# Performance work log

Hardware: AMD Instinct MI355X
Metric: run time of the kernel (lower is better)

Reference implementation:

```python
import jax, jax.numpy as jnp
import numpy as np

N_NODES = 50000
N_EDGES = 400000


def setup_inputs() -> dict:
    key = jax.random.key(0)
    ks = jax.random.split(key, 8)
    d_in, d_hid, d_out = 512, 512, 256
    feats = jax.random.normal(ks[0], (N_NODES, d_in), dtype=jnp.float32)
    src = jax.random.randint(ks[1], (N_EDGES,), 0, N_NODES, dtype=jnp.int32)
    dst = jax.random.randint(ks[2], (N_EDGES,), 0, N_NODES, dtype=jnp.int32)
    # Glorot-ish scaled weights so activations stay O(1)
    W0 = jax.random.normal(ks[3], (d_in, d_hid), dtype=jnp.float32) / np.sqrt(d_in)
    b0 = jnp.zeros((d_hid,), jnp.float32)
    W1 = jax.random.normal(ks[4], (d_hid, d_hid), dtype=jnp.float32) / np.sqrt(d_hid)
    b1 = jnp.zeros((d_hid,), jnp.float32)
    W2 = jax.random.normal(ks[5], (d_hid, d_out), dtype=jnp.float32) / np.sqrt(d_hid)
    b2 = jnp.zeros((d_out,), jnp.float32)
    return {"feats": feats, "src": src, "dst": dst,
            "W0": W0, "b0": b0, "W1": W1, "b1": b1, "W2": W2, "b2": b2}


def _sage_conv_gcn(h, src, dst, W, b, deg):
    # DGL SAGEConv aggregator_type='gcn':
    # h_neigh[v] = (sum_{u->v} h[u] + h[v]) / (in_deg(v) + 1); out = h_neigh @ W + b
    agg = jax.ops.segment_sum(h[src], dst, num_segments=h.shape[0])  # [N, d]
    h_neigh = (agg + h) / (deg[:, None] + 1.0)
    return h_neigh @ W + b


def reference(feats, src, dst, W0, b0, W1, b1, W2, b2):
    N = feats.shape[0]
    deg = jax.ops.segment_sum(jnp.ones((src.shape[0],), feats.dtype), dst,
                              num_segments=N)  # in-degree per node
    h = jax.nn.relu(_sage_conv_gcn(feats, src, dst, W0, b0, deg))  # dropout p=0, norm none
    h = jax.nn.relu(_sage_conv_gcn(h, src, dst, W1, b1, deg))
    h = _sage_conv_gcn(h, src, dst, W2, b2, deg)  # final layer: no activation
    return h
```

## Files before the change

kernel.cpp:

```cpp
#include <hip/hip_runtime.h>
#include <stdint.h>

#define N_NODES 50000
#define N_EDGES 400000
#define MPAD    50048
#define SCAN_B  49

typedef __bf16 bf16x8 __attribute__((ext_vector_type(8)));
typedef float  f32x4  __attribute__((ext_vector_type(4)));
typedef unsigned short ushort_t;
typedef unsigned int   uint_t;

__device__ __forceinline__ ushort_t f2b(float f){
    uint_t x = __float_as_uint(f);
    x += 0x7FFFu + ((x >> 16) & 1u);
    return (ushort_t)(x >> 16);
}
__device__ __forceinline__ float b2f(ushort_t h){
    return __uint_as_float(((uint_t)h) << 16);
}

__device__ __forceinline__ int xcd_swz(int orig, int nwg){
    int q = nwg >> 3, r = nwg & 7;
    int xcd = orig & 7, idx = orig >> 3;
    int base = (xcd < r) ? xcd * (q + 1) : r * (q + 1) + (xcd - r) * q;
    return base + idx;
}

__global__ void zero_two(int* a, int* b, int n){
    int i = blockIdx.x * blockDim.x + threadIdx.x;
    if (i < n){ a[i] = 0; b[i] = 0; }
}

__global__ void hist_kernel(const int* __restrict__ dst, int* __restrict__ deg, int E){
    int i = blockIdx.x * blockDim.x + threadIdx.x;
    if (i < E) atomicAdd(&deg[dst[i]], 1);
}

__global__ __launch_bounds__(1024) void blk_scan_kernel(
        const int* __restrict__ deg, int* __restrict__ offs,
        int* __restrict__ bsum, int n){
    __shared__ int buf[1024];
    const int t = threadIdx.x, b = blockIdx.x;
    const int i = b * 1024 + t;
    int v = (i < n) ? deg[i] : 0;
    buf[t] = v; __syncthreads();
    for (int off = 1; off < 1024; off <<= 1){
        int x = (t >= off) ? buf[t - off] : 0;
        __syncthreads();
        buf[t] += x;
        __syncthreads();
    }
    if (i < n) offs[i] = buf[t] - v;
    if (t == 1023) bsum[b] = buf[1023];
}

__global__ void bsum_scan_kernel(int* __restrict__ bsum, int nb){
    int t = threadIdx.x;
    int orig = (t < nb) ? bsum[t] : 0;
    int v = orig;
    #pragma unroll
    for (int off = 1; off < 64; off <<= 1){
        int x = __shfl_up(v, off, 64);
        if (t >= off) v += x;
    }
    if (t < nb) bsum[t] = v - orig;
}

__global__ __launch_bounds__(1024) void add_off_kernel(
        int* __restrict__ offs, const int* __restrict__ bsum, int n){
    int i = blockIdx.x * 1024 + threadIdx.x;
    if (i < n) offs[i] += bsum[blockIdx.x];
    if (i == 0) offs[n] = N_EDGES;
}

__global__ void fill_kernel(const int* __restrict__ src, const int* __restrict__ dst,
                            const int* __restrict__ offs, int* __restrict__ cursor,
                            int* __restrict__ nbr, int E){
    int i = blockIdx.x * blockDim.x + threadIdx.x;
    if (i < E){
        int d = dst[i];
        int p = atomicAdd(&cursor[d], 1);
        nbr[offs[d] + p] = src[i];
    }
}

__global__ void wtrans_kernel(const float* __restrict__ W, ushort_t* __restrict__ Wt,
                              int K, int N){
    int i = blockIdx.x * blockDim.x + threadIdx.x;
    if (i < K * N){
        int n = i / K, k = i - n * K;
        Wt[i] = f2b(W[k * N + n]);
    }
}

__device__ __forceinline__ void load16(const void* g, void* l){
    __builtin_amdgcn_global_load_lds((const __attribute__((address_space(1))) void*)g,
                                     (__attribute__((address_space(3))) void*)l, 16, 0, 0);
}

__global__ __launch_bounds__(256, 4) void gemm128_bt(const ushort_t* __restrict__ A,
                                                     const ushort_t* __restrict__ Bt,
                                                     ushort_t* __restrict__ C,
                                                     int NBN, int N, int K){
    __shared__ ushort_t As[128 * 64];
    __shared__ ushort_t Bs[128 * 64];
    const int tid  = threadIdx.x, lane = tid & 63, wave = tid >> 6;
    const int wg = xcd_swz(blockIdx.x, gridDim.x);
    const int bm = wg / NBN, bn = wg - bm * NBN;
    const int fr = lane & 15;
    const int wm = (wave >> 1) * 64, wn = (wave & 1) * 64;
    f32x4 acc[4][4] = {};

    for (int kt = 0; kt < K; kt += 64){
        __syncthreads();
        #pragma unroll
        for (int i = 0; i < 4; i++){
            int s = tid + i * 256;
            int row = s >> 3, p = s & 7, c = p ^ (row & 7);
            load16(A + (size_t)(bm * 128 + row) * K + kt + c * 8,
                   (char*)As + s * 16);
        }
        #pragma unroll
        for (int i = 0; i < 4; i++){
            int s = tid + i * 256;
            int row = s >> 3, p = s & 7, c = p ^ (row & 7);
            load16(Bt + (size_t)(bn * 128 + row) * K + kt + c * 8,
                   (char*)Bs + s * 16);
        }
        __syncthreads();
        #pragma unroll
        for (int ks = 0; ks < 2; ks++){
            const int c = (lane >> 4) + ks * 4;
            const int cx = c ^ (fr & 7);
            bf16x8 af[4], bf[4];
            #pragma unroll
            for (int t = 0; t < 4; t++)
                af[t] = *(const bf16x8*)(const void*)(As + (wm + t * 16 + fr) * 64 + cx * 8);
            #pragma unroll
            for (int t = 0; t < 4; t++)
                bf[t] = *(const bf16x8*)(const void*)(Bs + (wn + t * 16 + fr) * 64 + cx * 8);
            #pragma unroll
            for (int tm = 0; tm < 4; tm++)
                #pragma unroll
                for (int tn = 0; tn < 4; tn++)
                    acc[tm][tn] = __builtin_amdgcn_mfma_f32_16x16x32_bf16(
                                      af[tm], bf[tn], acc[tm][tn], 0, 0, 0);
        }
    }
    const int r0 = (lane >> 4) * 4, c0 = lane & 15;
    #pragma unroll
    for (int tm = 0; tm < 4; tm++){
        #pragma unroll
        for (int tn = 0; tn < 4; tn++){
            int rbase = bm * 128 + wm + tm * 16 + r0;
            int cidx  = bn * 128 + wn + tn * 16 + c0;
            #pragma unroll
            for (int reg = 0; reg < 4; reg++)
                C[(size_t)(rbase + reg) * N + cidx] = f2b(acc[tm][tn][reg]);
        }
    }
}

__global__ __launch_bounds__(256, 3) void gemm128_a32(const float* __restrict__ A,
                                                      const ushort_t* __restrict__ Bt,
                                                      ushort_t* __restrict__ C,
                                                      int K){
    __shared__ ushort_t As[128 * 64];
    __shared__ ushort_t Bs[128 * 64];
    const int tid  = threadIdx.x, lane = tid & 63, wave = tid >> 6;
    const int wg = xcd_swz(blockIdx.x, gridDim.x);
    const int bm = wg >> 2, bn = wg & 3;
    const int fr = lane & 15;
    const int wm = (wave >> 1) * 64, wn = (wave & 1) * 64;
    f32x4 acc[4][4] = {};

    for (int kt = 0; kt < K; kt += 64){
        __syncthreads();
        float4 x[4], y[4];
        #pragma unroll
        for (int i = 0; i < 4; i++){
            int s = tid + i * 256;
            int row = s >> 3, p = s & 7, c = p ^ (row & 7);
            int grow = bm * 128 + row;
            if (grow < N_NODES){
                const float* pp = A + (size_t)grow * K + kt + c * 8;
                x[i] = *(const float4*)(const void*)pp;
                y[i] = *(const float4*)(const void*)(pp + 4);
            } else {
                x[i] = make_float4(0.f, 0.f, 0.f, 0.f);
                y[i] = make_float4(0.f, 0.f, 0.f, 0.f);
            }
        }
        #pragma unroll
        for (int i = 0; i < 4; i++){
            int s = tid + i * 256;
            int row = s >> 3, p = s & 7, c = p ^ (row & 7);
            load16(Bt + (size_t)(bn * 128 + row) * K + kt + c * 8,
                   (char*)Bs + s * 16);
        }
        #pragma unroll
        for (int i = 0; i < 4; i++){
            int s = tid + i * 256;
            uint4 o;
            o.x = (uint_t)f2b(x[i].x) | ((uint_t)f2b(x[i].y) << 16);
            o.y = (uint_t)f2b(x[i].z) | ((uint_t)f2b(x[i].w) << 16);
            o.z = (uint_t)f2b(y[i].x) | ((uint_t)f2b(y[i].y) << 16);
            o.w = (uint_t)f2b(y[i].z) | ((uint_t)f2b(y[i].w) << 16);
            *(uint4*)(void*)((char*)As + s * 16) = o;
        }
        __syncthreads();
        #pragma unroll
        for (int ks = 0; ks < 2; ks++){
            const int c = (lane >> 4) + ks * 4;
            const int cx = c ^ (fr & 7);
            bf16x8 af[4], bf[4];
            #pragma unroll
            for (int t = 0; t < 4; t++)
                af[t] = *(const bf16x8*)(const void*)(As + (wm + t * 16 + fr) * 64 + cx * 8);
            #pragma unroll
            for (int t = 0; t < 4; t++)
                bf[t] = *(const bf16x8*)(const void*)(Bs + (wn + t * 16 + fr) * 64 + cx * 8);
            #pragma unroll
            for (int tm = 0; tm < 4; tm++)
                #pragma unroll
                for (int tn = 0; tn < 4; tn++)
                    acc[tm][tn] = __builtin_amdgcn_mfma_f32_16x16x32_bf16(
                                      af[tm], bf[tn], acc[tm][tn], 0, 0, 0);
        }
    }
    const int r0 = (lane >> 4) * 4, c0 = lane & 15;
    #pragma unroll
    for (int tm = 0; tm < 4; tm++){
        #pragma unroll
        for (int tn = 0; tn < 4; tn++){
            int rbase = bm * 128 + wm + tm * 16 + r0;
            int cidx  = bn * 128 + wn + tn * 16 + c0;
            #pragma unroll
            for (int reg = 0; reg < 4; reg++)
                C[(size_t)(rbase + reg) * 512 + cidx] = f2b(acc[tm][tn][reg]);
        }
    }
}

__device__ __forceinline__ void acc4(float* a, uint2 y){
    a[0] += b2f((ushort_t)(y.x & 0xffff)); a[1] += b2f((ushort_t)(y.x >> 16));
    a[2] += b2f((ushort_t)(y.y & 0xffff)); a[3] += b2f((ushort_t)(y.y >> 16));
}

__global__ __launch_bounds__(512) void agg_relu_kernel(
        const ushort_t* __restrict__ Y, const int* __restrict__ offs,
        const int* __restrict__ nbr, const float* __restrict__ bias,
        ushort_t* __restrict__ H){
    const int lane = threadIdx.x & 63, wv = threadIdx.x >> 6;
    const int v   = blockIdx.x * 4 + (wv >> 1);
    const int off = (wv & 1) * 256 + lane * 4;
    float a[4];
    {   uint2 y = *(const uint2*)(const void*)(Y + (size_t)v * 512 + off);
        a[0] = b2f((ushort_t)(y.x & 0xffff)); a[1] = b2f((ushort_t)(y.x >> 16));
        a[2] = b2f((ushort_t)(y.y & 0xffff)); a[3] = b2f((ushort_t)(y.y >> 16)); }
    const int beg = offs[v], end = offs[v + 1];
    int i = beg;
    for (; i + 8 <= end; i += 8){
        uint2 yy[8];
        #pragma unroll
        for (int j = 0; j < 8; j++){
            int u = nbr[i + j];
            yy[j] = *(const uint2*)(const void*)(Y + (size_t)u * 512 + off);
        }
        #pragma unroll
        for (int j = 0; j < 8; j++) acc4(a, yy[j]);
    }
    for (; i + 4 <= end; i += 4){
        uint2 yy[4];
        #pragma unroll
        for (int j = 0; j < 4; j++){
            int u = nbr[i + j];
            yy[j] = *(const uint2*)(const void*)(Y + (size_t)u * 512 + off);
        }
        #pragma unroll
        for (int j = 0; j < 4; j++) acc4(a, yy[j]);
    }
    for (; i < end; i++){
        int u = nbr[i];
        uint2 y = *(const uint2*)(const void*)(Y + (size_t)u * 512 + off);
        acc4(a, y);
    }
    const float inv = 1.0f / (float)(end - beg + 1);
    float4 bb = ((const float4*)bias)[(wv & 1) * 64 + lane];
    float r[4];
    r[0] = a[0]*inv + bb.x; r[1] = a[1]*inv + bb.y;
    r[2] = a[2]*inv + bb.z; r[3] = a[3]*inv + bb.w;
    #pragma unroll
    for (int j = 0; j < 4; j++) r[j] = r[j] > 0.f ? r[j] : 0.f;
    uint2 o;
    o.x = (uint_t)f2b(r[0]) | ((uint_t)f2b(r[1]) << 16);
    o.y = (uint_t)f2b(r[2]) | ((uint_t)f2b(r[3]) << 16);
    *(uint2*)(void*)(H + (size_t)v * 512 + off) = o;
}

__global__ __launch_bounds__(256) void agg_out_kernel(
        const ushort_t* __restrict__ Y, const int* __restrict__ offs,
        const int* __restrict__ nbr, const float* __restrict__ bias,
        float* __restrict__ out){
    const int lane = threadIdx.x & 63, wave = threadIdx.x >> 6;
    const int v = blockIdx.x * 4 + wave;
    const int off = lane * 4;
    float a[4];
    {   uint2 y = *(const uint2*)(const void*)(Y + (size_t)v * 256 + off);
        a[0] = b2f((ushort_t)(y.x & 0xffff)); a[1] = b2f((ushort_t)(y.x >> 16));
        a[2] = b2f((ushort_t)(y.y & 0xffff)); a[3] = b2f((ushort_t)(y.y >> 16)); }
    const int beg = offs[v], end = offs[v + 1];
    int i = beg;
    for (; i + 8 <= end; i += 8){
        uint2 yy[8];
        #pragma unroll
        for (int j = 0; j < 8; j++){
            int u = nbr[i + j];
            yy[j] = *(const uint2*)(const void*)(Y + (size_t)u * 256 + off);
        }
        #pragma unroll
        for (int j = 0; j < 8; j++) acc4(a, yy[j]);
    }
    for (; i + 4 <= end; i += 4){
        uint2 yy[4];
        #pragma unroll
        for (int j = 0; j < 4; j++){
            int u = nbr[i + j];
            yy[j] = *(const uint2*)(const void*)(Y + (size_t)u * 256 + off);
        }
        #pragma unroll
        for (int j = 0; j < 4; j++) acc4(a, yy[j]);
    }
    for (; i < end; i++){
        int u = nbr[i];
        uint2 y = *(const uint2*)(const void*)(Y + (size_t)u * 256 + off);
        acc4(a, y);
    }
    const float inv = 1.0f / (float)(end - beg + 1);
    float4 bb = ((const float4*)bias)[lane];
    float4 r;
    r.x = a[0]*inv + bb.x; r.y = a[1]*inv + bb.y;
    r.z = a[2]*inv + bb.z; r.w = a[3]*inv + bb.w;
    ((float4*)out)[v * 64 + lane] = r;
}

extern "C" void kernel_launch(void* const* d_in, const int* in_sizes, int n_in,
                              void* d_out, int out_size, void* d_ws, size_t ws_size,
                              hipStream_t stream) {
    const float* feats = (const float*)d_in[0];
    const int*   src   = (const int*)  d_in[1];
    const int*   dst   = (const int*)  d_in[2];
    const float* W0    = (const float*)d_in[3];
    const float* b0    = (const float*)d_in[4];
    const float* W1    = (const float*)d_in[5];
    const float* b1    = (const float*)d_in[6];
    const float* W2    = (const float*)d_in[7];
    const float* b2    = (const float*)d_in[8];
    float* out = (float*)d_out;

    char* w = (char*)d_ws;
    ushort_t* Abuf = (ushort_t*)w;  w += (size_t)MPAD * 512 * 2;
    ushort_t* Ybuf = (ushort_t*)w;  w += (size_t)MPAD * 512 * 2;
    ushort_t* W0t  = (ushort_t*)w;  w += 512 * 512 * 2;
    ushort_t* W1t  = (ushort_t*)w;  w += 512 * 512 * 2;
    ushort_t* W2t  = (ushort_t*)w;  w += 256 * 512 * 2;
    int* deg    = (int*)w;          w += 50048 * 4;
    int* offs   = (int*)w;          w += 50056 * 4;
    int* cursor = (int*)w;          w += 50048 * 4;
    int* nbr    = (int*)w;          w += (size_t)N_EDGES * 4;
    int* bsum   = (int*)w;          w += 64 * 4;

    zero_two<<<(N_NODES + 255) / 256, 256, 0, stream>>>(deg, cursor, N_NODES);
    hist_kernel<<<(N_EDGES + 255) / 256, 256, 0, stream>>>(dst, deg, N_EDGES);
    blk_scan_kernel<<<SCAN_B, 1024, 0, stream>>>(deg, offs, bsum, N_NODES);
    bsum_scan_kernel<<<1, 64, 0, stream>>>(bsum, SCAN_B);
    add_off_kernel<<<SCAN_B, 1024, 0, stream>>>(offs, bsum, N_NODES);
    fill_kernel<<<(N_EDGES + 255) / 256, 256, 0, stream>>>(src, dst, offs, cursor, nbr, N_EDGES);

    wtrans_kernel<<<(512 * 512 + 255) / 256, 256, 0, stream>>>(W0, W0t, 512, 512);
    wtrans_kernel<<<(512 * 512 + 255) / 256, 256, 0, stream>>>(W1, W1t, 512, 512);
    wtrans_kernel<<<(512 * 256 + 255) / 256, 256, 0, stream>>>(W2, W2t, 512, 256);

    const int g01 = (MPAD / 128) * 4;
    const int g2  = (MPAD / 128) * 2;

    gemm128_a32<<<g01, 256, 0, stream>>>(feats, W0t, Ybuf, 512);
    agg_relu_kernel<<<N_NODES / 4, 512, 0, stream>>>(Ybuf, offs, nbr, b0, Abuf);
    gemm128_bt<<<g01, 256, 0, stream>>>(Abuf, W1t, Ybuf, 4, 512, 512);
    agg_relu_kernel<<<N_NODES / 4, 512, 0, stream>>>(Ybuf, offs, nbr, b1, Abuf);
    gemm128_bt<<<g2, 256, 0, stream>>>(Abuf, W2t, Ybuf, 2, 256, 512);
    agg_out_kernel<<<N_NODES / 4, 256, 0, stream>>>(Ybuf, offs, nbr, b2, out);
}
```

Baseline: 496.6 us.

## Widen aggregation loads to 16 bytes, tile weight transpose, raise GEMM occupancy

The ReLU aggregation kernel now has one wave cover a whole 512-wide node row, with each lane loading 8 bf16 values (uint4) instead of 4. That halves the number of gather instructions per neighbour and the waves per node. The weight transpose now goes through a padded 32x32 shared-memory tile so both its reads and writes are coalesced. The first-layer GEMM's launch-bounds occupancy hint is raised from 3 to 4, which may limit registers and cause spills.

```diff
diff --git a/kernel.cpp b/kernel.cpp
--- a/kernel.cpp
+++ b/kernel.cpp
@@ -85,13 +85,20 @@
     }
 }
 
-__global__ void wtrans_kernel(const float* __restrict__ W, ushort_t* __restrict__ Wt,
-                              int K, int N){
-    int i = blockIdx.x * blockDim.x + threadIdx.x;
-    if (i < K * N){
-        int n = i / K, k = i - n * K;
-        Wt[i] = f2b(W[k * N + n]);
-    }
+__global__ __launch_bounds__(256) void wtrans_kernel(const float* __restrict__ W,
+                                                     ushort_t* __restrict__ Wt,
+                                                     int K, int N){
+    __shared__ float t[32][33];
+    const int bx = blockIdx.x * 32;
+    const int by = blockIdx.y * 32;
+    const int x = threadIdx.x & 31, y = threadIdx.x >> 5;
+    #pragma unroll
+    for (int j = 0; j < 32; j += 8)
+        t[y + j][x] = W[(size_t)(by + y + j) * N + bx + x];
+    __syncthreads();
+    #pragma unroll
+    for (int j = 0; j < 32; j += 8)
+        Wt[(size_t)(bx + y + j) * K + by + x] = f2b(t[x][y + j]);
 }
 
 __device__ __forceinline__ void load16(const void* g, void* l){
@@ -162,7 +169,7 @@
     }
 }
 
-__global__ __launch_bounds__(256, 3) void gemm128_a32(const float* __restrict__ A,
+__global__ __launch_bounds__(256, 4) void gemm128_a32(const float* __restrict__ A,
                                                       const ushort_t* __restrict__ Bt,
                                                       ushort_t* __restrict__ C,
                                                       int K){
@@ -243,60 +250,73 @@
     }
 }
 
+__device__ __forceinline__ void acc8(float* a, uint4 y){
+    a[0] += b2f((ushort_t)(y.x & 0xffff)); a[1] += b2f((ushort_t)(y.x >> 16));
+    a[2] += b2f((ushort_t)(y.y & 0xffff)); a[3] += b2f((ushort_t)(y.y >> 16));
+    a[4] += b2f((ushort_t)(y.z & 0xffff)); a[5] += b2f((ushort_t)(y.z >> 16));
+    a[6] += b2f((ushort_t)(y.w & 0xffff)); a[7] += b2f((ushort_t)(y.w >> 16));
+}
 __device__ __forceinline__ void acc4(float* a, uint2 y){
     a[0] += b2f((ushort_t)(y.x & 0xffff)); a[1] += b2f((ushort_t)(y.x >> 16));
     a[2] += b2f((ushort_t)(y.y & 0xffff)); a[3] += b2f((ushort_t)(y.y >> 16));
 }
 
-__global__ __launch_bounds__(512) void agg_relu_kernel(
+__global__ __launch_bounds__(256) void agg_relu_kernel(
         const ushort_t* __restrict__ Y, const int* __restrict__ offs,
         const int* __restrict__ nbr, const float* __restrict__ bias,
         ushort_t* __restrict__ H){
-    const int lane = threadIdx.x & 63, wv = threadIdx.x >> 6;
-    const int v   = blockIdx.x * 4 + (wv >> 1);
-    const int off = (wv & 1) * 256 + lane * 4;
-    float a[4];
-    {   uint2 y = *(const uint2*)(const void*)(Y + (size_t)v * 512 + off);
+    const int lane = threadIdx.x & 63, wave = threadIdx.x >> 6;
+    const int v = blockIdx.x * 4 + wave;
+    const int off = lane * 8;
+    float a[8];
+    {   uint4 y = *(const uint4*)(const void*)(Y + (size_t)v * 512 + off);
         a[0] = b2f((ushort_t)(y.x & 0xffff)); a[1] = b2f((ushort_t)(y.x >> 16));
-        a[2] = b2f((ushort_t)(y.y & 0xffff)); a[3] = b2f((ushort_t)(y.y >> 16)); }
+        a[2] = b2f((ushort_t)(y.y & 0xffff)); a[3] = b2f((ushort_t)(y.y >> 16));
+        a[4] = b2f((ushort_t)(y.z & 0xffff)); a[5] = b2f((ushort_t)(y.z >> 16));
+        a[6] = b2f((ushort_t)(y.w & 0xffff)); a[7] = b2f((ushort_t)(y.w >> 16)); }
     const int beg = offs[v], end = offs[v + 1];
     int i = beg;
     for (; i + 8 <= end; i += 8){
-        uint2 yy[8];
+        uint4 yy[8];
         #pragma unroll
         for (int j = 0; j < 8; j++){
             int u = nbr[i + j];
-            yy[j] = *(const uint2*)(const void*)(Y + (size_t)u * 512 + off);
-        }
-        #pragma unroll
-        for (int j = 0; j < 8; j++) acc4(a, yy[j]);
+            yy[j] = *(const uint4*)(const void*)(Y + (size_t)u * 512 + off);
+        }
+        #pragma unroll
+        for (int j = 0; j < 8; j++) acc8(a, yy[j]);
     }
     for (; i + 4 <= end; i += 4){
-        uint2 yy[4];
+        uint4 yy[4];
         #pragma unroll
         for (int j = 0; j < 4; j++){
             int u = nbr[i + j];
-            yy[j] = *(const uint2*)(const void*)(Y + (size_t)u * 512 + off);
-        }
-        #pragma unroll
-        for (int j = 0; j < 4; j++) acc4(a, yy[j]);
+            yy[j] = *(const uint4*)(const void*)(Y + (size_t)u * 512 + off);
+        }
+        #pragma unroll
+        for (int j = 0; j < 4; j++) acc8(a, yy[j]);
     }
     for (; i < end; i++){
         int u = nbr[i];
-        uint2 y = *(const uint2*)(const void*)(Y + (size_t)u * 512 + off);
-        acc4(a, y);
+        uint4 y = *(const uint4*)(const void*)(Y + (size_t)u * 512 + off);
+        acc8(a, y);
     }
     const float inv = 1.0f / (float)(end - beg + 1);
-    float4 bb = ((const float4*)bias)[(wv & 1) * 64 + lane];
-    float r[4];
-    r[0] = a[0]*inv + bb.x; r[1] = a[1]*inv + bb.y;
-    r[2] = a[2]*inv + bb.z; r[3] = a[3]*inv + bb.w;
-    #pragma unroll
-    for (int j = 0; j < 4; j++) r[j] = r[j] > 0.f ? r[j] : 0.f;
-    uint2 o;
+    float4 bb0 = ((const float4*)bias)[lane * 2];
+    float4 bb1 = ((const float4*)bias)[lane * 2 + 1];
+    float r[8];
+    r[0] = a[0]*inv + bb0.x; r[1] = a[1]*inv + bb0.y;
+    r[2] = a[2]*inv + bb0.z; r[3] = a[3]*inv + bb0.w;
+    r[4] = a[4]*inv + bb1.x; r[5] = a[5]*inv + bb1.y;
+    r[6] = a[6]*inv + bb1.z; r[7] = a[7]*inv + bb1.w;
+    #pragma unroll
+    for (int j = 0; j < 8; j++) r[j] = r[j] > 0.f ? r[j] : 0.f;
+    uint4 o;
     o.x = (uint_t)f2b(r[0]) | ((uint_t)f2b(r[1]) << 16);
     o.y = (uint_t)f2b(r[2]) | ((uint_t)f2b(r[3]) << 16);
-    *(uint2*)(void*)(H + (size_t)v * 512 + off) = o;
+    o.z = (uint_t)f2b(r[4]) | ((uint_t)f2b(r[5]) << 16);
+    o.w = (uint_t)f2b(r[6]) | ((uint_t)f2b(r[7]) << 16);
+    *(uint4*)(void*)(H + (size_t)v * 512 + off) = o;
 }
 
 __global__ __launch_bounds__(256) void agg_out_kernel(
@@ -378,17 +398,21 @@
     add_off_kernel<<<SCAN_B, 1024, 0, stream>>>(offs, bsum, N_NODES);
     fill_kernel<<<(N_EDGES + 255) / 256, 256, 0, stream>>>(src, dst, offs, cursor, nbr, N_EDGES);
 
-    wtrans_kernel<<<(512 * 512 + 255) / 256, 256, 0, stream>>>(W0, W0t, 512, 512);
-    wtrans_kernel<<<(512 * 512 + 255) / 256, 256, 0, stream>>>(W1, W1t, 512, 512);
-    wtrans_kernel<<<(512 * 256 + 255) / 256, 256, 0, stream>>>(W2, W2t, 512, 256);
+    {
+        dim3 gt0(512 / 32, 512 / 32);
+        wtrans_kernel<<<gt0, 256, 0, stream>>>(W0, W0t, 512, 512);
+        wtrans_kernel<<<gt0, 256, 0, stream>>>(W1, W1t, 512, 512);
+        dim3 gt2(256 / 32, 512 / 32);
+        wtrans_kernel<<<gt2, 256, 0, stream>>>(W2, W2t, 512, 256);
+    }
 
     const int g01 = (MPAD / 128) * 4;
     const int g2  = (MPAD / 128) * 2;
 
     gemm128_a32<<<g01, 256, 0, stream>>>(feats, W0t, Ybuf, 512);
-    agg_relu_kernel<<<N_NODES / 4, 512, 0, stream>>>(Ybuf, offs, nbr, b0, Abuf);
+    agg_relu_kernel<<<N_NODES / 4, 256, 0, stream>>>(Ybuf, offs, nbr, b0, Abuf);
     gemm128_bt<<<g01, 256, 0, stream>>>(Abuf, W1t, Ybuf, 4, 512, 512);
-    agg_relu_kernel<<<N_NODES / 4, 512, 0, stream>>>(Ybuf, offs, nbr, b1, Abuf);
+    agg_relu_kernel<<<N_NODES / 4, 256, 0, stream>>>(Ybuf, offs, nbr, b1, Abuf);
     gemm128_bt<<<g2, 256, 0, stream>>>(Abuf, W2t, Ybuf, 2, 256, 512);
     agg_out_kernel<<<N_NODES / 4, 256, 0, stream>>>(Ybuf, offs, nbr, b2, out);
 }
```

After: 480.6 us. -3.2%, faster.
